# Performance work log

Measured on AMD Instinct MI355X. Metric: run time of the kernel, lower is better.

Reference implementation:

```python
import jax, jax.numpy as jnp
import numpy as np

B, N, E, D = 8, 10000, 160000, 256
H = D // 2
SLOPE = 0.2  # LeakyReLU negative slope


def setup_inputs() -> dict:
    key = jax.random.key(0)
    ks = jax.random.split(key, 8)
    node_feats = jax.random.normal(ks[0], (B, N, D), dtype=jnp.float32)
    edge_attr = jax.random.uniform(ks[1], (E, 1), dtype=jnp.float32)
    W1 = jax.random.normal(ks[2], (2 * D, H), dtype=jnp.float32) * 0.05
    b1 = jnp.zeros((H,), dtype=jnp.float32)
    W2 = jax.random.normal(ks[3], (H, 1), dtype=jnp.float32) * 0.05
    b2 = jnp.zeros((1,), dtype=jnp.float32)
    edge_index = jax.random.randint(ks[4], (2, E), 0, N, dtype=jnp.int64)
    valid_masks = jax.random.randint(ks[5], (B, N), 0, 2).astype(bool)
    return {"node_feats": node_feats, "edge_attr": edge_attr, "W1": W1, "b1": b1,
            "W2": W2, "b2": b2, "edge_index": edge_index, "valid_masks": valid_masks}


def reference(node_feats, edge_attr, W1, b1, W2, b2, edge_index, valid_masks):
    # node_feats: [B,N,D]; edge_index: [2,E] shared across batch
    d = node_feats.shape[-1]
    src, dst = edge_index[0], edge_index[1]
    # cat([src_feats, dst_feats]) @ W1 == src @ W1[:d] + dst @ W1[d:]
    # Project per-node first, then gather per-edge: avoids the [B,E,2D] concat.
    ps = jnp.einsum('bnd,dh->bnh', node_feats, W1[:d])   # [B,N,H]
    pd = jnp.einsum('bnd,dh->bnh', node_feats, W1[d:])   # [B,N,H]
    h = ps[:, src] + pd[:, dst] + b1                      # [B,E,H]
    h = jnp.where(h >= 0, h, SLOPE * h)                   # LeakyReLU(0.2)
    scores = jnp.einsum('beh,h->be', h, W2[:, 0]) + b2[0]  # [B,E]
    scores = scores * edge_attr[:, 0]                     # edge_attr multiplies pre-softmax
    w = jax.nn.softmax(scores, axis=1)                    # global softmax over all edges
    # sparse_coo(edge_index, w) @ node_feats: out[src[e]] += w[e] * feats[dst[e]]
    msg = w[..., None] * node_feats[:, dst]               # [B,E,D]
    n = node_feats.shape[1]
    agg = jax.vmap(lambda m: jax.ops.segment_sum(m, src, num_segments=n))(msg)  # [B,N,D]
    mask = valid_masks.astype(node_feats.dtype)           # [B,N]
    cnt = mask.sum(axis=1)                                # [B]
    masked_mean = (agg * mask[..., None]).sum(axis=1) / jnp.maximum(cnt, 1.0)[:, None]
    full_mean = agg.mean(axis=1)
    graph_feats = jnp.where((cnt > 0)[:, None], masked_mean, full_mean)  # [B,D]
    return graph_feats, w
```

## Files before the change

### kernel.cpp

```cpp
#include <hip/hip_runtime.h>
#include <hip/hip_bf16.h>
#include <hip/hip_fp16.h>

#define B_ 8
#define N_ 10000
#define E_ 160000
#define D_ 256
#define H_ 128
#define SLOPE 0.2f
#define NCHUNK 100

#define NB_ 64
#define EPB_ (E_ / NB_)
#define BINS_ 256
#define NPB_ (N_ / 16)
#define SUBS_ 8

#define SB_ 256
#define SEB_ (E_ / SB_)

typedef __attribute__((ext_vector_type(8))) _Float16 v8h;
typedef __attribute__((ext_vector_type(4))) _Float16 v4h;
typedef __attribute__((ext_vector_type(2))) _Float16 v2h;
typedef __attribute__((ext_vector_type(4))) float f32x4;

static __device__ __forceinline__ float dot2f(v2h a, v2h b, float c) {
#if __has_builtin(__builtin_amdgcn_fdot2)
    return __builtin_amdgcn_fdot2(a, b, c, false);
#else
    return fmaf((float)a.y, (float)b.y, fmaf((float)a.x, (float)b.x, c));
#endif
}

static __device__ __forceinline__ void block_flags(const int* __restrict__ eidx_raw,
                                                   const unsigned int* __restrict__ mask32,
                                                   int tid, int* sfl) {
    if (tid < 64) {
        unsigned long long oddnz = __ballot(eidx_raw[2 * tid + 1] != 0);
        unsigned long long mgt1  = __ballot(mask32[tid] > 1u);
        if (tid == 0) {
            sfl[0] = (oddnz == 0ull) ? 1 : 0;
            sfl[1] = (mgt1 != 0ull) ? 1 : 0;
        }
    }
    __syncthreads();
}

__global__ __launch_bounds__(256) void kprep(const int* __restrict__ eidx_raw,
                                             const unsigned char* __restrict__ mask8,
                                             const unsigned int* __restrict__ mask32,
                                             const float* __restrict__ W1,
                                             const float* __restrict__ b1,
                                             const float* __restrict__ W2,
                                             int* __restrict__ ce,
                                             unsigned char* __restrict__ cmT,
                                             __half* __restrict__ Wt,
                                             __half* __restrict__ b1h,
                                             __half* __restrict__ w2h,
                                             int* __restrict__ cnti,
                                             int* __restrict__ hpart) {
    const int tid = threadIdx.x;
    __shared__ int sfl[2];
    __shared__ int scnt[8];

    if (blockIdx.x < 1250) {
        if (tid < 8) scnt[tid] = 0;
        block_flags(eidx_raw, mask32, tid, sfl);
        const int f_e = sfl[0], f_m = sfl[1];
        const int i = blockIdx.x * 256 + tid;
        if (i < 2 * E_) ce[i] = f_e ? eidx_raw[2 * i] : eidx_raw[i];
        if (i < B_ * N_) {
            unsigned char v = f_m ? (unsigned char)(mask8[i] != 0)
                                  : (unsigned char)(mask32[i] != 0u);
            const int b = i / N_;
            const int n = i - b * N_;
            cmT[n * 8 + b] = v;
            if (v) atomicAdd(&scnt[b], 1);
        }
        if (i < 2 * 256 * 128) {
            const int f = i & 127;
            const int row = i >> 7;
            const int c = row >> 8, k = row & 255;
            Wt[((c * 128 + f) * 256) + k] = __float2half(W1[row * 128 + f]);
        }
        if (i < 128) {
            b1h[i] = __float2half(b1[i]);
            w2h[i] = __float2half(W2[i]);
        }
        __syncthreads();
        if (tid < 8 && scnt[tid]) atomicAdd(&cnti[tid], scnt[tid]);
    } else {
        block_flags(eidx_raw, mask32, tid, sfl);
        const int f_e = sfl[0];
        __shared__ int h[BINS_];
        h[tid] = 0;
        __syncthreads();
        const int hb = blockIdx.x - 1250;
        const int base = hb * EPB_;
        for (int i = tid; i < EPB_; i += 256) {
            const int e = base + i;
            const int s = f_e ? eidx_raw[2 * e] : eidx_raw[e];
            const int d = f_e ? eidx_raw[2 * (E_ + e)] : eidx_raw[E_ + e];
            const int bin = (d / NPB_) * 16 + s / NPB_;
            atomicAdd(&h[bin], 1);
        }
        __syncthreads();
        hpart[hb * BINS_ + tid] = h[tid];
    }
}

__global__ __launch_bounds__(256) void kprefix(const int* __restrict__ hpart,
                                               int* __restrict__ offsetG,
                                               int* __restrict__ bstart) {
    __shared__ int cnt[BINS_];
    __shared__ int excl[BINS_];
    const int bin = threadIdx.x;
    int c = 0;
    for (int b = 0; b < NB_; b++) c += hpart[b * BINS_ + bin];
    cnt[bin] = c;
    __syncthreads();
    if (bin == 0) {
        int r = 0;
        for (int i = 0; i < BINS_; i++) { excl[i] = r; r += cnt[i]; }
    }
    __syncthreads();
    if ((bin & 15) == 0) bstart[bin >> 4] = excl[bin];
    if (bin == 0) bstart[16] = E_;
    int run = excl[bin];
    for (int b = 0; b < NB_; b++) {
        offsetG[b * BINS_ + bin] = run;
        run += hpart[b * BINS_ + bin];
    }
}

__global__ __launch_bounds__(256) void k1_mfma(const float* __restrict__ X,
                                               const __half* __restrict__ Wt,
                                               __half* __restrict__ ps,
                                               __half* __restrict__ pd,
                                               const int* __restrict__ ce,
                                               const int* __restrict__ offsetG,
                                               int4* __restrict__ esort,
                                               int* __restrict__ rank) {
    const int tid = threadIdx.x;
    __shared__ __align__(16) char smem[64 * 136 * 2];

    if (blockIdx.x >= 1250) {
        int* loc = (int*)smem;
        const int sb = blockIdx.x - 1250;
        loc[tid] = offsetG[sb * BINS_ + tid];
        __syncthreads();
        const int base = sb * EPB_;
        for (int i = tid; i < EPB_; i += 256) {
            const int e = base + i;
            const int s = ce[e], d = ce[E_ + e];
            const int bin = (d / NPB_) * 16 + s / NPB_;
            const int pos = atomicAdd(&loc[bin], 1);
            esort[pos] = make_int4(s, d, e, 0);
            rank[e] = pos;
        }
        return;
    }

    const int rb = blockIdx.x;
    const int wave = tid >> 6, lane = tid & 63;
    const int quad = lane >> 4, l16 = lane & 15;
    _Float16* Xs = (_Float16*)smem;
    _Float16* T  = (_Float16*)smem;

    f32x4 acc[2][2][4];
#pragma unroll
    for (int c = 0; c < 2; c++)
#pragma unroll
        for (int i = 0; i < 2; i++)
#pragma unroll
            for (int j = 0; j < 4; j++) acc[c][i][j] = (f32x4){0.f, 0.f, 0.f, 0.f};

    const int row_base = rb * 64;
    const int sr = tid >> 3;
    const int sc = (tid & 7) * 4;

    const float* xsrc  = &X[(size_t)(row_base + sr) * 256 + sc];
    const float* xsrc2 = xsrc + 32 * 256;
    const __half* wbase = &Wt[((size_t)(wave * 32 + l16)) * 256 + quad * 8];

    float4 xa, xb;
    v8h wcur[2][2], wnxt[2][2];

    xa = *(const float4*)(xsrc);
    xb = *(const float4*)(xsrc2);
#pragma unroll
    for (int cb = 0; cb < 2; cb++)
#pragma unroll
        for (int ft = 0; ft < 2; ft++)
            wcur[cb][ft] = *(const v8h*)(wbase + (size_t)(cb * 128 + ft * 16) * 256);
    {
        v4h pa = {(_Float16)xa.x, (_Float16)xa.y, (_Float16)xa.z, (_Float16)xa.w};
        v4h pb = {(_Float16)xb.x, (_Float16)xb.y, (_Float16)xb.z, (_Float16)xb.w};
        *(v4h*)&Xs[sr * 40 + sc] = pa;
        *(v4h*)&Xs[(sr + 32) * 40 + sc] = pb;
    }
    __syncthreads();

    for (int kc = 0; kc < 8; ++kc) {
        const int cur = kc & 1;
        if (kc < 7) {
            xa = *(const float4*)(xsrc + (kc + 1) * 32);
            xb = *(const float4*)(xsrc2 + (kc + 1) * 32);
#pragma unroll
            for (int cb = 0; cb < 2; cb++)
#pragma unroll
                for (int ft = 0; ft < 2; ft++)
                    wnxt[cb][ft] = *(const v8h*)(wbase + (size_t)(cb * 128 + ft * 16) * 256 + (kc + 1) * 32);
        }
#pragma unroll
        for (int nt = 0; nt < 4; ++nt) {
            v8h xf = *(v8h*)&Xs[cur * (64 * 40) + (nt * 16 + l16) * 40 + quad * 8];
            acc[0][0][nt] = __builtin_amdgcn_mfma_f32_16x16x32_f16(wcur[0][0], xf, acc[0][0][nt], 0, 0, 0);
            acc[0][1][nt] = __builtin_amdgcn_mfma_f32_16x16x32_f16(wcur[0][1], xf, acc[0][1][nt], 0, 0, 0);
            acc[1][0][nt] = __builtin_amdgcn_mfma_f32_16x16x32_f16(wcur[1][0], xf, acc[1][0][nt], 0, 0, 0);
            acc[1][1][nt] = __builtin_amdgcn_mfma_f32_16x16x32_f16(wcur[1][1], xf, acc[1][1][nt], 0, 0, 0);
        }
        if (kc < 7) {
            const int nb = (cur ^ 1) * (64 * 40);
            v4h pa = {(_Float16)xa.x, (_Float16)xa.y, (_Float16)xa.z, (_Float16)xa.w};
            v4h pb = {(_Float16)xb.x, (_Float16)xb.y, (_Float16)xb.z, (_Float16)xb.w};
            *(v4h*)&Xs[nb + sr * 40 + sc] = pa;
            *(v4h*)&Xs[nb + (sr + 32) * 40 + sc] = pb;
#pragma unroll
            for (int cb = 0; cb < 2; cb++)
#pragma unroll
                for (int ft = 0; ft < 2; ft++)
                    wcur[cb][ft] = wnxt[cb][ft];
        }
        __syncthreads();
    }

#pragma unroll
    for (int cb = 0; cb < 2; ++cb) {
        if (cb) __syncthreads();
#pragma unroll
        for (int nt = 0; nt < 4; ++nt)
#pragma unroll
            for (int ft = 0; ft < 2; ++ft) {
                f32x4 a = acc[cb][ft][nt];
                v4h h = {(_Float16)a.x, (_Float16)a.y, (_Float16)a.z, (_Float16)a.w};
                *(v4h*)&T[(nt * 16 + l16) * 136 + wave * 32 + ft * 16 + quad * 4] = h;
            }
        __syncthreads();
        __half* outp = cb ? pd : ps;
#pragma unroll
        for (int pass = 0; pass < 4; ++pass) {
            const int r = pass * 16 + (tid >> 4);
            const int f8 = (tid & 15) * 8;
            const int R = row_base + r;
            const int b = R / N_;
            const int n = R - b * N_;
            *(float4*)(outp + ((size_t)(n * 8 + b)) * 128 + f8) =
                *(const float4*)&T[r * 136 + f8];
        }
    }
}

__global__ __launch_bounds__(256) void k2_scores(const __half* __restrict__ ps,
                                                 const __half* __restrict__ pd,
                                                 const int4* __restrict__ esort,
                                                 const __half* __restrict__ b1h,
                                                 const __half* __restrict__ w2h,
                                                 const float* __restrict__ b2,
                                                 const float* __restrict__ eattr,
                                                 float* __restrict__ scS) {
    const int tid = threadIdx.x;
    const int wave = tid >> 6;
    const int lane = tid & 63;
    const int bid = blockIdx.x;
    const int lb = (bid & 7) * 2500 + (bid >> 3);
    const int e0 = lb * 8 + wave * 2;

    const int b = lane >> 3;
    const int hi = (lane & 7) * 16;

    v2h b1p[8], w2p[8];
    {
        const v2h* bp = (const v2h*)(b1h + hi);
        const v2h* wp = (const v2h*)(w2h + hi);
#pragma unroll
        for (int j = 0; j < 8; j++) { b1p[j] = bp[j]; w2p[j] = wp[j]; }
    }
    const float bias2 = b2[0];
    const v2h slp = {(_Float16)SLOPE, (_Float16)SLOPE};

#pragma unroll
    for (int q = 0; q < 2; q++) {
        const int e = e0 + q;
        const int4 er = esort[e];
        const int src = er.x, dst = er.y, orig = er.z;

        const float4* aps = (const float4*)&ps[((size_t)src * 8 + b) * 128 + hi];
        const float4* apd = (const float4*)&pd[((size_t)dst * 8 + b) * 128 + hi];
        float4 rs[2] = {aps[0], aps[1]};
        float4 rd[2] = {apd[0], apd[1]};
        const v2h* sv = (const v2h*)rs;
        const v2h* dv = (const v2h*)rd;

        float acc = 0.f;
#pragma unroll
        for (int j = 0; j < 8; j++) {
            v2h x = sv[j] + dv[j] + b1p[j];
            v2h l = __builtin_elementwise_max(x, x * slp);
            acc = dot2f(l, w2p[j], acc);
        }
        acc += __shfl_xor(acc, 1);
        acc += __shfl_xor(acc, 2);
        acc += __shfl_xor(acc, 4);

        if ((lane & 7) == 0) {
            scS[(size_t)e * 8 + b] = (acc + bias2) * eattr[orig];
        }
    }
}

__global__ __launch_bounds__(256) void k3s_stats(const float* __restrict__ scS,
                                                 float* __restrict__ pmax,
                                                 double* __restrict__ psum) {
    const int tid = threadIdx.x;
    const int wave = tid >> 6, lane = tid & 63;
    const int base = blockIdx.x * SEB_;

    float fm[8];
#pragma unroll
    for (int j = 0; j < 8; j++) fm[j] = -3.4e38f;
    for (int i = tid; i < SEB_; i += 256) {
        const float4* s4 = (const float4*)&scS[(size_t)(base + i) * 8];
        float4 a = s4[0], b = s4[1];
        fm[0] = fmaxf(fm[0], a.x); fm[1] = fmaxf(fm[1], a.y);
        fm[2] = fmaxf(fm[2], a.z); fm[3] = fmaxf(fm[3], a.w);
        fm[4] = fmaxf(fm[4], b.x); fm[5] = fmaxf(fm[5], b.y);
        fm[6] = fmaxf(fm[6], b.z); fm[7] = fmaxf(fm[7], b.w);
    }
#pragma unroll
    for (int k = 1; k <= 32; k <<= 1)
#pragma unroll
        for (int j = 0; j < 8; j++) fm[j] = fmaxf(fm[j], __shfl_xor(fm[j], k));
    __shared__ float lmax[4][8];
    if (lane == 0)
#pragma unroll
        for (int j = 0; j < 8; j++) lmax[wave][j] = fm[j];
    __syncthreads();
    float m[8];
#pragma unroll
    for (int j = 0; j < 8; j++)
        m[j] = fmaxf(fmaxf(lmax[0][j], lmax[1][j]), fmaxf(lmax[2][j], lmax[3][j]));

    double s[8];
#pragma unroll
    for (int j = 0; j < 8; j++) s[j] = 0.0;
    for (int i = tid; i < SEB_; i += 256) {
        const float4* s4 = (const float4*)&scS[(size_t)(base + i) * 8];
        float4 a = s4[0], b = s4[1];
        s[0] += (double)expf(a.x - m[0]); s[1] += (double)expf(a.y - m[1]);
        s[2] += (double)expf(a.z - m[2]); s[3] += (double)expf(a.w - m[3]);
        s[4] += (double)expf(b.x - m[4]); s[5] += (double)expf(b.y - m[5]);
        s[6] += (double)expf(b.z - m[6]); s[7] += (double)expf(b.w - m[7]);
    }
#pragma unroll
    for (int k = 1; k <= 32; k <<= 1)
#pragma unroll
        for (int j = 0; j < 8; j++) s[j] += __shfl_xor(s[j], k);
    __shared__ double lsum[4][8];
    if (lane == 0)
#pragma unroll
        for (int j = 0; j < 8; j++) lsum[wave][j] = s[j];
    __syncthreads();
    if (tid < 8) {
        pmax[blockIdx.x * 8 + tid] = m[tid];
        psum[blockIdx.x * 8 + tid] = lsum[0][tid] + lsum[1][tid] + lsum[2][tid] + lsum[3][tid];
    }
}

static __device__ __forceinline__ void stats_combine(const float* __restrict__ pmax,
                                                     const double* __restrict__ psum,
                                                     int tid, float* smx, float* sinvx) {
    if (tid < 64) {
        float mc[SB_ / 64][8];
        float v[8];
#pragma unroll
        for (int j = 0; j < 8; j++) v[j] = -3.4e38f;
#pragma unroll
        for (int g = 0; g < SB_ / 64; g++) {
            const float4* p4 = (const float4*)&pmax[(g * 64 + tid) * 8];
            float4 a = p4[0], b = p4[1];
            mc[g][0] = a.x; mc[g][1] = a.y; mc[g][2] = a.z; mc[g][3] = a.w;
            mc[g][4] = b.x; mc[g][5] = b.y; mc[g][6] = b.z; mc[g][7] = b.w;
#pragma unroll
            for (int j = 0; j < 8; j++) v[j] = fmaxf(v[j], mc[g][j]);
        }
#pragma unroll
        for (int k = 1; k <= 32; k <<= 1)
#pragma unroll
            for (int j = 0; j < 8; j++) v[j] = fmaxf(v[j], __shfl_xor(v[j], k));
        double z[8];
#pragma unroll
        for (int j = 0; j < 8; j++) z[j] = 0.0;
#pragma unroll
        for (int g = 0; g < SB_ / 64; g++)
#pragma unroll
            for (int j = 0; j < 8; j++)
                z[j] += psum[(g * 64 + tid) * 8 + j] * (double)expf(mc[g][j] - v[j]);
#pragma unroll
        for (int k = 1; k <= 32; k <<= 1)
#pragma unroll
            for (int j = 0; j < 8; j++) z[j] += __shfl_xor(z[j], k);
        if (tid == 0)
#pragma unroll
            for (int j = 0; j < 8; j++) { smx[j] = v[j]; sinvx[j] = (float)(1.0 / z[j]); }
    }
}

__global__ __launch_bounds__(256) void k3ef(const int4* __restrict__ esort,
                                            const float* __restrict__ scS,
                                            const unsigned char* __restrict__ cmT,
                                            const float* __restrict__ pmax,
                                            const double* __restrict__ psum,
                                            const int* __restrict__ bstart,
                                            const int* __restrict__ rank,
                                            float* __restrict__ Wpf,
                                            float* __restrict__ Wpm,
                                            float* __restrict__ wout) {
    const int tid = threadIdx.x;
    __shared__ float smx[8], sinvx[8];
    __shared__ float lWf[NPB_ * 8];
    __shared__ float lWm[NPB_ * 8];

    stats_combine(pmax, psum, tid, smx, sinvx);

    if (blockIdx.x >= 16 * SUBS_) {
        __syncthreads();
        const int e = (blockIdx.x - 16 * SUBS_) * 256 + tid;
        const int p = rank[e];
        const float4* s4 = (const float4*)&scS[(size_t)p * 8];
        float4 a = s4[0], b = s4[1];
        float wv[8];
        wv[0] = expf(a.x - smx[0]) * sinvx[0]; wv[1] = expf(a.y - smx[1]) * sinvx[1];
        wv[2] = expf(a.z - smx[2]) * sinvx[2]; wv[3] = expf(a.w - smx[3]) * sinvx[3];
        wv[4] = expf(b.x - smx[4]) * sinvx[4]; wv[5] = expf(b.y - smx[5]) * sinvx[5];
        wv[6] = expf(b.z - smx[6]) * sinvx[6]; wv[7] = expf(b.w - smx[7]) * sinvx[7];
#pragma unroll
        for (int j = 0; j < 8; j++) wout[(size_t)j * E_ + e] = wv[j];
        return;
    }

    const int bucket = blockIdx.x / SUBS_;
    const int sub = blockIdx.x % SUBS_;

    for (int i = tid; i < NPB_ * 8; i += 256) { lWf[i] = 0.f; lWm[i] = 0.f; }
    __syncthreads();

    float m[8], inv[8];
#pragma unroll
    for (int j = 0; j < 8; j++) { m[j] = smx[j]; inv[j] = sinvx[j]; }

    const int bs = bstart[bucket], be = bstart[bucket + 1];
    const int len = be - bs;
    const int s0 = bs + (int)((long long)len * sub / SUBS_);
    const int s1 = bs + (int)((long long)len * (sub + 1) / SUBS_);
    const int nbase = bucket * NPB_;

    for (int p = s0 + tid; p < s1; p += 256) {
        const int4 er = esort[p];
        const int src = er.x;
        const int rel = er.y - nbase;
        const float4* s4 = (const float4*)&scS[(size_t)p * 8];
        float4 a = s4[0], b = s4[1];
        float wv[8];
        wv[0] = expf(a.x - m[0]) * inv[0]; wv[1] = expf(a.y - m[1]) * inv[1];
        wv[2] = expf(a.z - m[2]) * inv[2]; wv[3] = expf(a.w - m[3]) * inv[3];
        wv[4] = expf(b.x - m[4]) * inv[4]; wv[5] = expf(b.y - m[5]) * inv[5];
        wv[6] = expf(b.z - m[6]) * inv[6]; wv[7] = expf(b.w - m[7]) * inv[7];
        const unsigned long long mm = *(const unsigned long long*)&cmT[src * 8];
        float* lf = &lWf[rel * 8];
        float* lm = &lWm[rel * 8];
#pragma unroll
        for (int j = 0; j < 8; j++) {
            atomicAdd(&lf[j], wv[j]);
            if ((mm >> (8 * j)) & 1ull) atomicAdd(&lm[j], wv[j]);
        }
    }
    __syncthreads();

    float* of = Wpf + ((size_t)bucket * SUBS_ + sub) * (NPB_ * 8);
    float* om = Wpm + ((size_t)bucket * SUBS_ + sub) * (NPB_ * 8);
    for (int i = tid; i < NPB_ * 8; i += 256) { of[i] = lWf[i]; om[i] = lWm[i]; }
}

__global__ __launch_bounds__(256) void k3g_reduce(const float* __restrict__ Wpf,
                                                  const float* __restrict__ Wpm,
                                                  float* __restrict__ WfT,
                                                  float* __restrict__ WmT) {
    const int i = blockIdx.x * 256 + threadIdx.x;
    if (i >= N_ * 8) return;
    const int n = i >> 3, b = i & 7;
    const int bucket = n / NPB_;
    const int rel = n - bucket * NPB_;
    float sf = 0.f, sm = 0.f;
#pragma unroll
    for (int sub = 0; sub < SUBS_; sub++) {
        const size_t off = ((size_t)bucket * SUBS_ + sub) * (NPB_ * 8) + rel * 8 + b;
        sf += Wpf[off];
        sm += Wpm[off];
    }
    WfT[i] = sf;
    WmT[i] = sm;
}

__global__ __launch_bounds__(256) void k4b_wsum(const float* __restrict__ X,
                                                const float* __restrict__ WmT,
                                                const float* __restrict__ WfT,
                                                float* __restrict__ gpart) {
    const int c = blockIdx.x;
    const int b = blockIdx.y;
    const int tx = threadIdx.x & 63;
    const int ty = threadIdx.x >> 6;
    const int npc = N_ / NCHUNK;
    const int n0 = c * npc;

    const float4* X4 = (const float4*)(X + (size_t)b * N_ * 256);
    float4 am = {0.f, 0.f, 0.f, 0.f};
    float4 af = {0.f, 0.f, 0.f, 0.f};

    for (int n = n0 + ty; n < n0 + npc; n += 4) {
        float wm = WmT[n * 8 + b];
        float wf = WfT[n * 8 + b];
        float4 v = X4[(size_t)n * 64 + tx];
        am.x = fmaf(wm, v.x, am.x); am.y = fmaf(wm, v.y, am.y);
        am.z = fmaf(wm, v.z, am.z); am.w = fmaf(wm, v.w, am.w);
        af.x = fmaf(wf, v.x, af.x); af.y = fmaf(wf, v.y, af.y);
        af.z = fmaf(wf, v.z, af.z); af.w = fmaf(wf, v.w, af.w);
    }

    __shared__ float4 red[256];
    red[threadIdx.x] = am;
    __syncthreads();
    if (ty == 0) {
        float4 r1 = red[tx + 64], r2 = red[tx + 128], r3 = red[tx + 192];
        am.x += r1.x + r2.x + r3.x; am.y += r1.y + r2.y + r3.y;
        am.z += r1.z + r2.z + r3.z; am.w += r1.w + r2.w + r3.w;
    }
    __syncthreads();
    red[threadIdx.x] = af;
    __syncthreads();
    if (ty == 0) {
        float4 r1 = red[tx + 64], r2 = red[tx + 128], r3 = red[tx + 192];
        af.x += r1.x + r2.x + r3.x; af.y += r1.y + r2.y + r3.y;
        af.z += r1.z + r2.z + r3.z; af.w += r1.w + r2.w + r3.w;
        float4* gp4 = (float4*)gpart;
        gp4[((c * 2 + 0) * 8 + b) * 64 + tx] = am;
        gp4[((c * 2 + 1) * 8 + b) * 64 + tx] = af;
    }
}

__global__ __launch_bounds__(256) void k5_final(const float* __restrict__ gpart,
                                                const int* __restrict__ cnti,
                                                float* __restrict__ gf) {
    const int b = blockIdx.x;
    const int d = threadIdx.x;
    float sm = 0.f, sf = 0.f;
    for (int c = 0; c < NCHUNK; c++) {
        sm += gpart[((c * 2 + 0) * 8 + b) * 256 + d];
        sf += gpart[((c * 2 + 1) * 8 + b) * 256 + d];
    }
    const float cn = (float)cnti[b];
    gf[b * 256 + d] = (cn > 0.f) ? (sm / cn) : (sf / (float)N_);
}

static inline char* align16(char* p) {
    return (char*)(((uintptr_t)p + 15) & ~(uintptr_t)15);
}

extern "C" void kernel_launch(void* const* d_in, const int* in_sizes, int n_in,
                              void* d_out, int out_size, void* d_ws, size_t ws_size,
                              hipStream_t stream) {
    const float* X     = (const float*)d_in[0];
    const float* eattr = (const float*)d_in[1];
    const float* W1    = (const float*)d_in[2];
    const float* b1    = (const float*)d_in[3];
    const float* W2    = (const float*)d_in[4];
    const float* b2    = (const float*)d_in[5];
    const int*   eidx_raw = (const int*)d_in[6];
    const unsigned char* mask8 = (const unsigned char*)d_in[7];
    const unsigned int*  mask32 = (const unsigned int*)d_in[7];

    float* out  = (float*)d_out;
    float* gf   = out;
    float* wout = out + 2048;

    char* cur = (char*)d_ws;
    __half* ps_h = (__half*)cur;             cur += (size_t)N_ * 8 * 128 * 2;
    __half* pd_h = (__half*)cur;             cur += (size_t)N_ * 8 * 128 * 2;
    __half* Wt   = (__half*)cur;             cur += 2 * 128 * 256 * 2;
    int* ce      = (int*)cur;                cur += 2 * E_ * 4;
    unsigned char* cmT = (unsigned char*)cur; cur += N_ * 8;
    cur = align16(cur);
    int* cnti    = (int*)cur;                cur += 8 * 4;
    cur = align16(cur);
    float* pmax  = (float*)cur;              cur += SB_ * 8 * 4;
    cur = align16(cur);
    double* psum = (double*)cur;             cur += SB_ * 8 * 8;
    float* gpart = (float*)cur;              cur += NCHUNK * 2 * 8 * 256 * 4;
    int* hpart   = (int*)cur;                cur += NB_ * BINS_ * 4;
    int* offsetG = (int*)cur;                cur += NB_ * BINS_ * 4;
    int* bstart  = (int*)cur;                cur += 32 * 4;
    cur = align16(cur);
    int4* esort  = (int4*)cur;               cur += (size_t)E_ * 16;
    int* rankB   = (int*)cur;                cur += E_ * 4;
    __half* b1h  = (__half*)cur;             cur += 128 * 2;
    __half* w2h  = (__half*)cur;             cur += 128 * 2;
    cur = align16(cur);
    float* scS   = (float*)cur;              cur += (size_t)E_ * 8 * 4;

    char* ocur = (char*)d_ws;
    float* Wpf = (float*)ocur;               ocur += (size_t)16 * SUBS_ * NPB_ * 8 * 4;
    float* Wpm = (float*)ocur;               ocur += (size_t)16 * SUBS_ * NPB_ * 8 * 4;
    float* WfT = (float*)ocur;               ocur += N_ * 8 * 4;
    float* WmT = (float*)ocur;               ocur += N_ * 8 * 4;

    hipMemsetAsync(cnti, 0, 8 * sizeof(int), stream);
    hipLaunchKernelGGL(kprep, dim3(1250 + NB_), dim3(256), 0, stream,
                       eidx_raw, mask8, mask32, W1, b1, W2,
                       ce, cmT, Wt, b1h, w2h, cnti, hpart);
    hipLaunchKernelGGL(kprefix, dim3(1), dim3(256), 0, stream, hpart, offsetG, bstart);
    hipLaunchKernelGGL(k1_mfma, dim3(1250 + NB_), dim3(256), 0, stream,
                       X, Wt, ps_h, pd_h, ce, offsetG, esort, rankB);
    hipLaunchKernelGGL(k2_scores, dim3(E_ / 8), dim3(256), 0, stream,
                       ps_h, pd_h, esort, b1h, w2h, b2, eattr, scS);
    hipLaunchKernelGGL(k3s_stats, dim3(SB_), dim3(256), 0, stream, scS, pmax, psum);
    hipLaunchKernelGGL(k3ef, dim3(16 * SUBS_ + E_ / 256), dim3(256), 0, stream,
                       esort, scS, cmT, pmax, psum, bstart, rankB, Wpf, Wpm, wout);
    hipLaunchKernelGGL(k3g_reduce, dim3((N_ * 8 + 255) / 256), dim3(256), 0, stream,
                       Wpf, Wpm, WfT, WmT);
    hipLaunchKernelGGL(k4b_wsum, dim3(NCHUNK, 8), dim3(256), 0, stream, X, WmT, WfT, gpart);
    hipLaunchKernelGGL(k5_final, dim3(8), dim3(256), 0, stream, gpart, cnti, gf);
}
```

Measured before the change: 276.7 us.

## Switch projections and scores from node-interleaved to batch-major layout

Stores the per-node projections ps/pd as [B][N][H] instead of [N][B][H], and the edge scores as [B][E] instead of [E][B]. The score kernel now pins each block to one batch and lets each group of 8 lanes handle a different edge. The stats and weight kernels read scores with a batch stride. The aim is to keep one batch's 2.5 MB projection slice cache-resident while edges are gathered. The cost is that each edge's sorted index record is now fetched once per batch instead of once overall, and the strided score reads replace float4 loads.

```diff
diff --git a/kernel.cpp b/kernel.cpp
--- a/kernel.cpp
+++ b/kernel.cpp
@@ -255,7 +255,7 @@
             const int R = row_base + r;
             const int b = R / N_;
             const int n = R - b * N_;
-            *(float4*)(outp + ((size_t)(n * 8 + b)) * 128 + f8) =
+            *(float4*)(outp + ((size_t)b * N_ + n) * 128 + f8) =
                 *(const float4*)&T[r * 136 + f8];
         }
     }
@@ -273,10 +273,9 @@
     const int wave = tid >> 6;
     const int lane = tid & 63;
     const int bid = blockIdx.x;
-    const int lb = (bid & 7) * 2500 + (bid >> 3);
-    const int e0 = lb * 8 + wave * 2;
-
-    const int b = lane >> 3;
+    const int batch = bid & 7;
+    const int e0 = (bid >> 3) * 64;
+
     const int hi = (lane & 7) * 16;
 
     v2h b1p[8], w2p[8];
@@ -289,14 +288,18 @@
     const float bias2 = b2[0];
     const v2h slp = {(_Float16)SLOPE, (_Float16)SLOPE};
 
+    const __half* psb = ps + (size_t)batch * N_ * 128;
+    const __half* pdb = pd + (size_t)batch * N_ * 128;
+    float* scb = scS + (size_t)batch * E_;
+
 #pragma unroll
     for (int q = 0; q < 2; q++) {
-        const int e = e0 + q;
+        const int e = e0 + wave * 16 + q * 8 + (lane >> 3);
         const int4 er = esort[e];
         const int src = er.x, dst = er.y, orig = er.z;
 
-        const float4* aps = (const float4*)&ps[((size_t)src * 8 + b) * 128 + hi];
-        const float4* apd = (const float4*)&pd[((size_t)dst * 8 + b) * 128 + hi];
+        const float4* aps = (const float4*)&psb[(size_t)src * 128 + hi];
+        const float4* apd = (const float4*)&pdb[(size_t)dst * 128 + hi];
         float4 rs[2] = {aps[0], aps[1]};
         float4 rd[2] = {apd[0], apd[1]};
         const v2h* sv = (const v2h*)rs;
@@ -314,7 +317,7 @@
         acc += __shfl_xor(acc, 4);
 
         if ((lane & 7) == 0) {
-            scS[(size_t)e * 8 + b] = (acc + bias2) * eattr[orig];
+            scb[e] = (acc + bias2) * eattr[orig];
         }
     }
 }
@@ -330,12 +333,10 @@
 #pragma unroll
     for (int j = 0; j < 8; j++) fm[j] = -3.4e38f;
     for (int i = tid; i < SEB_; i += 256) {
-        const float4* s4 = (const float4*)&scS[(size_t)(base + i) * 8];
-        float4 a = s4[0], b = s4[1];
-        fm[0] = fmaxf(fm[0], a.x); fm[1] = fmaxf(fm[1], a.y);
-        fm[2] = fmaxf(fm[2], a.z); fm[3] = fmaxf(fm[3], a.w);
-        fm[4] = fmaxf(fm[4], b.x); fm[5] = fmaxf(fm[5], b.y);
-        fm[6] = fmaxf(fm[6], b.z); fm[7] = fmaxf(fm[7], b.w);
+        const int p = base + i;
+#pragma unroll
+        for (int j = 0; j < 8; j++)
+            fm[j] = fmaxf(fm[j], scS[(size_t)j * E_ + p]);
     }
 #pragma unroll
     for (int k = 1; k <= 32; k <<= 1)
@@ -355,12 +356,10 @@
 #pragma unroll
     for (int j = 0; j < 8; j++) s[j] = 0.0;
     for (int i = tid; i < SEB_; i += 256) {
-        const float4* s4 = (const float4*)&scS[(size_t)(base + i) * 8];
-        float4 a = s4[0], b = s4[1];
-        s[0] += (double)expf(a.x - m[0]); s[1] += (double)expf(a.y - m[1]);
-        s[2] += (double)expf(a.z - m[2]); s[3] += (double)expf(a.w - m[3]);
-        s[4] += (double)expf(b.x - m[4]); s[5] += (double)expf(b.y - m[5]);
-        s[6] += (double)expf(b.z - m[6]); s[7] += (double)expf(b.w - m[7]);
+        const int p = base + i;
+#pragma unroll
+        for (int j = 0; j < 8; j++)
+            s[j] += (double)expf(scS[(size_t)j * E_ + p] - m[j]);
     }
 #pragma unroll
     for (int k = 1; k <= 32; k <<= 1)
@@ -437,15 +436,11 @@
         __syncthreads();
         const int e = (blockIdx.x - 16 * SUBS_) * 256 + tid;
         const int p = rank[e];
-        const float4* s4 = (const float4*)&scS[(size_t)p * 8];
-        float4 a = s4[0], b = s4[1];
-        float wv[8];
-        wv[0] = expf(a.x - smx[0]) * sinvx[0]; wv[1] = expf(a.y - smx[1]) * sinvx[1];
-        wv[2] = expf(a.z - smx[2]) * sinvx[2]; wv[3] = expf(a.w - smx[3]) * sinvx[3];
-        wv[4] = expf(b.x - smx[4]) * sinvx[4]; wv[5] = expf(b.y - smx[5]) * sinvx[5];
-        wv[6] = expf(b.z - smx[6]) * sinvx[6]; wv[7] = expf(b.w - smx[7]) * sinvx[7];
-#pragma unroll
-        for (int j = 0; j < 8; j++) wout[(size_t)j * E_ + e] = wv[j];
+#pragma unroll
+        for (int j = 0; j < 8; j++) {
+            const float v = scS[(size_t)j * E_ + p];
+            wout[(size_t)j * E_ + e] = expf(v - smx[j]) * sinvx[j];
+        }
         return;
     }
 
@@ -469,13 +464,10 @@
         const int4 er = esort[p];
         const int src = er.x;
         const int rel = er.y - nbase;
-        const float4* s4 = (const float4*)&scS[(size_t)p * 8];
-        float4 a = s4[0], b = s4[1];
         float wv[8];
-        wv[0] = expf(a.x - m[0]) * inv[0]; wv[1] = expf(a.y - m[1]) * inv[1];
-        wv[2] = expf(a.z - m[2]) * inv[2]; wv[3] = expf(a.w - m[3]) * inv[3];
-        wv[4] = expf(b.x - m[4]) * inv[4]; wv[5] = expf(b.y - m[5]) * inv[5];
-        wv[6] = expf(b.z - m[6]) * inv[6]; wv[7] = expf(b.w - m[7]) * inv[7];
+#pragma unroll
+        for (int j = 0; j < 8; j++)
+            wv[j] = expf(scS[(size_t)j * E_ + p] - m[j]) * inv[j];
         const unsigned long long mm = *(const unsigned long long*)&cmT[src * 8];
         float* lf = &lWf[rel * 8];
         float* lm = &lWm[rel * 8];
```

New measurement: 276.6 us. No clear change (-0.0%).
